# Kernel tuning notes

Measured on AMD Instinct MI355X. Metric: run time of the kernel, lower is better.

Reference implementation:

```python
import jax, jax.numpy as jnp
import numpy as np

B, S, D_IN, H, D_OUT = 2048, 16, 512, 1024, 64

def _lin_init(key, fan_in, fan_out):
    k1, k2 = jax.random.split(key)
    bound = 1.0 / np.sqrt(fan_in)
    W = jax.random.uniform(k1, (fan_in, fan_out), jnp.float32, -bound, bound)
    b = jax.random.uniform(k2, (fan_out,), jnp.float32, -bound, bound)
    return W, b

def setup_inputs() -> dict:
    key = jax.random.key(0)
    ks = jax.random.split(key, 7)
    x = jax.random.normal(ks[0], (B, S, D_IN), jnp.float32)
    Wi, bi = _lin_init(ks[1], D_IN, H)
    W1, b1 = _lin_init(ks[2], H, H)
    W2, b2 = _lin_init(ks[3], H, H)
    W3, b3 = _lin_init(ks[4], H, H)
    Wo1, bo1 = _lin_init(ks[5], H, H // 2)
    Wo2, bo2 = _lin_init(ks[6], H // 2, D_OUT)
    return {"x": x, "Wi": Wi, "bi": bi, "W1": W1, "b1": b1, "W2": W2, "b2": b2,
            "W3": W3, "b3": b3, "Wo1": Wo1, "bo1": bo1, "Wo2": Wo2, "bo2": bo2}

def reference(x, Wi, bi, W1, b1, W2, b2, W3, b3, Wo1, bo1, Wo2, bo2):
    seq_len = x.shape[1]
    dt = 1.0 / (seq_len - 1)  # t = linspace(0, 1, seq_len)

    def f(h):
        h = jax.nn.gelu(h @ W1 + b1, approximate=False)
        h = jax.nn.gelu(h @ W2 + b2, approximate=False)
        h = jax.nn.gelu(h @ W3 + b3, approximate=False)
        return h

    h0 = x[:, 0, :] @ Wi + bi  # [B, H]

    def rk4_38_step(h, _):  # torchdiffeq fixed-grid rk4 uses the 3/8 rule
        k1 = f(h)
        k2 = f(h + dt * k1 / 3.0)
        k3 = f(h + dt * (k2 - k1 / 3.0))
        k4 = f(h + dt * (k1 - k2 + k3))
        return h + dt * (k1 + 3.0 * k2 + 3.0 * k3 + k4) / 8.0, None

    h_final, _ = jax.lax.scan(rk4_38_step, h0, None, length=seq_len - 1)
    out = jax.nn.gelu(h_final @ Wo1 + bo1, approximate=False) @ Wo2 + bo2
    return out
```

## Files before the change

kernel.cpp:

```cpp
#include <hip/hip_runtime.h>
#include <hip/hip_bf16.h>
#include <math.h>

typedef __attribute__((ext_vector_type(8))) short bf16x8;
typedef __attribute__((ext_vector_type(4))) float f32x4;

#define EPI_T   0
#define EPI_H0  1
#define EPI_K1  2
#define EPI_K2  3
#define EPI_K3  4
#define EPI_K4  5
#define EPI_OUT 6

static __device__ __forceinline__ unsigned short f2bf(float f) {
  unsigned int u = __float_as_uint(f);
  u += 0x7FFFu + ((u >> 16) & 1u);
  return (unsigned short)(u >> 16);
}
static __device__ __forceinline__ float bf2f(unsigned short s) {
  return __uint_as_float(((unsigned int)s) << 16);
}
static __device__ __forceinline__ float gelu_f(float x) {
  return 0.5f * x * (1.0f + erff(x * 0.70710678118654752f));
}

typedef __attribute__((address_space(3))) unsigned int lds_u32;
typedef const __attribute__((address_space(1))) unsigned int glb_u32;
static __device__ __forceinline__ void gl_lds16(const unsigned short* g, unsigned short* l) {
  __builtin_amdgcn_global_load_lds((glb_u32*)g, (lds_u32*)l, 16, 0, 0);
}

template<int EPI>
__global__ __launch_bounds__(256, 2)
void gemm_k(const unsigned short* __restrict__ A,
            const unsigned short* __restrict__ Wt,
            const float* __restrict__ bias,
            void* __restrict__ outp,
            unsigned short* __restrict__ ob2,
            const float* __restrict__ hF,
            float* __restrict__ huF,
            const unsigned short* __restrict__ k1p,
            const unsigned short* __restrict__ k2p,
            float dt, int N, int K, int nwg)
{
  __shared__ __attribute__((aligned(16))) unsigned short As[3][64][128];

  const int bid = blockIdx.x;
  const int cpx = nwg >> 3;
  const int wid = (bid & 7) * cpx + (bid >> 3);
  const int nbx = N >> 6;
  const int bx = wid % nbx, by = wid / nbx;
  const int brow = by << 6, bcol = bx << 6;

  const int tid = threadIdx.x;
  const int lane = tid & 63;
  const int wv = tid >> 6;
  const int wr = wv >> 1, wc = wv & 1;
  const int l15 = lane & 15, l4 = lane >> 4;
  const int KT = K >> 7;

  f32x4 acc[2][2];
  const f32x4 zf = {0.f, 0.f, 0.f, 0.f};
#pragma unroll
  for (int m = 0; m < 2; ++m)
#pragma unroll
    for (int n = 0; n < 2; ++n) acc[m][n] = zf;

  const unsigned short* pB0 = Wt + (size_t)(bcol + wc * 32 + l15) * K + l4 * 8;
  const unsigned short* pB1 = pB0 + (size_t)16 * K;

  const int lrow = lane >> 4;
  auto STAGE = [&](int slot, int kt) {
    const int kof = kt << 7;
#pragma unroll
    for (int c = 0; c < 4; ++c) {
      const int r0 = wv * 16 + c * 4;
      const int sc = l15 ^ ((r0 + lrow) & 15);
      gl_lds16(A + (size_t)(brow + r0 + lrow) * K + kof + sc * 8, &As[slot][r0][0]);
    }
  };

  auto LOADB = [&](bf16x8 (&bg)[2][4], int kt) {
    const int kof = kt << 7;
#pragma unroll
    for (int ks = 0; ks < 4; ++ks) {
      bg[0][ks] = *(const bf16x8*)(pB0 + kof + ks * 32);
      bg[1][ks] = *(const bf16x8*)(pB1 + kof + ks * 32);
    }
  };

  auto COMP = [&](int slot, bf16x8 (&bg)[2][4]) {
    __builtin_amdgcn_s_setprio(1);
#pragma unroll
    for (int ks = 0; ks < 4; ++ks) {
      const int ch = ((ks * 4 + l4) ^ l15) * 8;
      bf16x8 af0 = *(const bf16x8*)&As[slot][wr * 32 + l15][ch];
      bf16x8 af1 = *(const bf16x8*)&As[slot][wr * 32 + 16 + l15][ch];
      acc[0][0] = __builtin_amdgcn_mfma_f32_16x16x32_bf16(af0, bg[0][ks], acc[0][0], 0, 0, 0);
      acc[0][1] = __builtin_amdgcn_mfma_f32_16x16x32_bf16(af0, bg[1][ks], acc[0][1], 0, 0, 0);
      acc[1][0] = __builtin_amdgcn_mfma_f32_16x16x32_bf16(af1, bg[0][ks], acc[1][0], 0, 0, 0);
      acc[1][1] = __builtin_amdgcn_mfma_f32_16x16x32_bf16(af1, bg[1][ks], acc[1][1], 0, 0, 0);
    }
    __builtin_amdgcn_s_setprio(0);
  };

  bf16x8 Bp[2][4], Bq[2][4];

  STAGE(0, 0);
  STAGE(1, 1);
  LOADB(Bp, 0);

  auto body = [&](int t, bf16x8 (&cur)[2][4], bf16x8 (&nxt)[2][4]) {
    if (t + 1 < KT) { asm volatile("s_waitcnt vmcnt(4)" ::: "memory"); }
    else            { asm volatile("s_waitcnt vmcnt(0)" ::: "memory"); }
    __builtin_amdgcn_s_barrier();
    __builtin_amdgcn_sched_barrier(0);
    if (t + 1 < KT) LOADB(nxt, t + 1);
    COMP(t % 3, cur);
    if (t + 2 < KT) STAGE((t + 2) % 3, t + 2);
  };

  for (int t = 0; t < KT; t += 2) {
    body(t, Bp, Bq);
    body(t + 1, Bq, Bp);
  }

  const float dt3 = dt * (1.f / 3.f), dt8 = dt * 0.125f, dt38 = dt * 0.375f;
#pragma unroll
  for (int n = 0; n < 2; ++n) {
    const int col = bcol + wc * 32 + n * 16 + l15;
    const float bv = bias[col];
#pragma unroll
    for (int m = 0; m < 2; ++m) {
      const int r0 = brow + wr * 32 + m * 16 + l4 * 4;
#pragma unroll
      for (int r = 0; r < 4; ++r) {
        const int row = r0 + r;
        const float a = acc[m][n][r] + bv;
        const size_t ix = (size_t)row * N + col;
        const size_t ih = (size_t)row * 1024 + col;
        if constexpr (EPI == EPI_T) {
          ((unsigned short*)outp)[ix] = f2bf(gelu_f(a));
        } else if constexpr (EPI == EPI_H0) {
          ((float*)outp)[ix] = a;
          ob2[ix] = f2bf(a);
        } else if constexpr (EPI == EPI_K1) {
          const float k1 = gelu_f(a);
          const float h = hF[ih];
          ((unsigned short*)outp)[ih] = f2bf(k1);
          huF[ih] = h + dt8 * k1;
          ob2[ih] = f2bf(h + dt3 * k1);
        } else if constexpr (EPI == EPI_K2) {
          const float k2 = gelu_f(a);
          const float h = hF[ih];
          const float k1 = bf2f(k1p[ih]);
          ((unsigned short*)outp)[ih] = f2bf(k2);
          huF[ih] += dt38 * k2;
          ob2[ih] = f2bf(h - dt3 * k1 + dt * k2);
        } else if constexpr (EPI == EPI_K3) {
          const float k3 = gelu_f(a);
          const float h = hF[ih];
          const float k1 = bf2f(k1p[ih]);
          const float k2 = bf2f(k2p[ih]);
          huF[ih] += dt38 * k3;
          ob2[ih] = f2bf(h + dt * (k1 - k2 + k3));
        } else if constexpr (EPI == EPI_K4) {
          const float k4 = gelu_f(a);
          const float hn = huF[ih] + dt8 * k4;
          ((float*)outp)[ih] = hn;
          ob2[ih] = f2bf(hn);
        } else {
          ((float*)outp)[ix] = a;
        }
      }
    }
  }
}

__global__ void transpose_k(const float* __restrict__ W, unsigned short* __restrict__ Wt,
                            int K, int N) {
  __shared__ float tile[32][33];
  const int n0 = blockIdx.x * 32, k0 = blockIdx.y * 32;
  const int lx = threadIdx.x, ly = threadIdx.y;
#pragma unroll
  for (int r = ly; r < 32; r += 8)
    tile[r][lx] = W[(size_t)(k0 + r) * N + n0 + lx];
  __syncthreads();
#pragma unroll
  for (int r = ly; r < 32; r += 8)
    Wt[(size_t)(n0 + r) * K + k0 + lx] = f2bf(tile[lx][r]);
}

__global__ void convx_k(const float* __restrict__ x, unsigned short* __restrict__ xb) {
  const int r = blockIdx.x;
  const int c = threadIdx.x << 3;
  const float* s = x + (size_t)r * 8192 + c;
  f32x4 u0 = *(const f32x4*)s;
  f32x4 u1 = *(const f32x4*)(s + 4);
  union { unsigned short q[8]; bf16x8 v; } t;
#pragma unroll
  for (int j = 0; j < 4; ++j) { t.q[j] = f2bf(u0[j]); t.q[4 + j] = f2bf(u1[j]); }
  *(bf16x8*)(xb + (size_t)r * 512 + c) = t.v;
}

template<int EPI>
static inline void G(hipStream_t st, const void* A, const unsigned short* Wt,
                     const float* bias, void* out, void* ob2,
                     const float* hF, float* huF,
                     const unsigned short* k1p, const unsigned short* k2p,
                     float dt, int N, int K) {
  const int nwg = (2048 / 64) * (N / 64);
  gemm_k<EPI><<<nwg, 256, 0, st>>>((const unsigned short*)A, Wt, bias, out,
                                   (unsigned short*)ob2, hF, huF, k1p, k2p, dt, N, K, nwg);
}

extern "C" void kernel_launch(void* const* d_in, const int* in_sizes, int n_in,
                              void* d_out, int out_size, void* d_ws, size_t ws_size,
                              hipStream_t stream) {
  const float* x   = (const float*)d_in[0];
  const float* Wi  = (const float*)d_in[1];
  const float* bi  = (const float*)d_in[2];
  const float* W1  = (const float*)d_in[3];
  const float* b1  = (const float*)d_in[4];
  const float* W2  = (const float*)d_in[5];
  const float* b2  = (const float*)d_in[6];
  const float* W3  = (const float*)d_in[7];
  const float* b3  = (const float*)d_in[8];
  const float* Wo1 = (const float*)d_in[9];
  const float* bo1 = (const float*)d_in[10];
  const float* Wo2 = (const float*)d_in[11];
  const float* bo2 = (const float*)d_in[12];

  char* ws = (char*)d_ws;
  unsigned short* Wti  = (unsigned short*)(ws + (0ull  << 20));
  unsigned short* Wt1  = (unsigned short*)(ws + (1ull  << 20));
  unsigned short* Wt2  = (unsigned short*)(ws + (3ull  << 20));
  unsigned short* Wt3  = (unsigned short*)(ws + (5ull  << 20));
  unsigned short* Wto1 = (unsigned short*)(ws + (7ull  << 20));
  unsigned short* Wto2 = (unsigned short*)(ws + (8ull  << 20));
  float*          h    = (float*)(ws + (9ull  << 20));
  float*          hu   = (float*)(ws + (17ull << 20));
  unsigned short* xb   = (unsigned short*)hu;
  unsigned short* k1b  = (unsigned short*)(ws + (25ull << 20));
  unsigned short* o1b  = k1b;
  unsigned short* k2b  = (unsigned short*)(ws + (29ull << 20));
  unsigned short* t1b  = (unsigned short*)(ws + (33ull << 20));
  unsigned short* t2b  = (unsigned short*)(ws + (37ull << 20));
  unsigned short* cA   = (unsigned short*)(ws + (41ull << 20));
  unsigned short* hb   = (unsigned short*)(ws + (45ull << 20));

  dim3 tb(32, 8);
  transpose_k<<<dim3(1024 / 32,  512 / 32), tb, 0, stream>>>(Wi,  Wti,  512, 1024);
  transpose_k<<<dim3(1024 / 32, 1024 / 32), tb, 0, stream>>>(W1,  Wt1, 1024, 1024);
  transpose_k<<<dim3(1024 / 32, 1024 / 32), tb, 0, stream>>>(W2,  Wt2, 1024, 1024);
  transpose_k<<<dim3(1024 / 32, 1024 / 32), tb, 0, stream>>>(W3,  Wt3, 1024, 1024);
  transpose_k<<<dim3( 512 / 32, 1024 / 32), tb, 0, stream>>>(Wo1, Wto1, 1024, 512);
  transpose_k<<<dim3(  64 / 32,  512 / 32), tb, 0, stream>>>(Wo2, Wto2,  512,  64);
  convx_k<<<2048, 64, 0, stream>>>(x, xb);

  const float dt = 1.0f / 15.0f;

  G<EPI_H0>(stream, xb, Wti, bi, h, hb, nullptr, nullptr, nullptr, nullptr, dt, 1024, 512);

  for (int s = 0; s < 15; ++s) {
    G<EPI_T >(stream, hb,  Wt1, b1, t1b, nullptr, nullptr, nullptr, nullptr, nullptr, dt, 1024, 1024);
    G<EPI_T >(stream, t1b, Wt2, b2, t2b, nullptr, nullptr, nullptr, nullptr, nullptr, dt, 1024, 1024);
    G<EPI_K1>(stream, t2b, Wt3, b3, k1b, cA, h, hu, nullptr, nullptr, dt, 1024, 1024);
    G<EPI_T >(stream, cA,  Wt1, b1, t1b, nullptr, nullptr, nullptr, nullptr, nullptr, dt, 1024, 1024);
    G<EPI_T >(stream, t1b, Wt2, b2, t2b, nullptr, nullptr, nullptr, nullptr, nullptr, dt, 1024, 1024);
    G<EPI_K2>(stream, t2b, Wt3, b3, k2b, cA, h, hu, k1b, nullptr, dt, 1024, 1024);
    G<EPI_T >(stream, cA,  Wt1, b1, t1b, nullptr, nullptr, nullptr, nullptr, nullptr, dt, 1024, 1024);
    G<EPI_T >(stream, t1b, Wt2, b2, t2b, nullptr, nullptr, nullptr, nullptr, nullptr, dt, 1024, 1024);
    G<EPI_K3>(stream, t2b, Wt3, b3, nullptr, cA, h, hu, k1b, k2b, dt, 1024, 1024);
    G<EPI_T >(stream, cA,  Wt1, b1, t1b, nullptr, nullptr, nullptr, nullptr, nullptr, dt, 1024, 1024);
    G<EPI_T >(stream, t1b, Wt2, b2, t2b, nullptr, nullptr, nullptr, nullptr, nullptr, dt, 1024, 1024);
    G<EPI_K4>(stream, t2b, Wt3, b3, h, hb, nullptr, hu, nullptr, nullptr, dt, 1024, 1024);
  }

  G<EPI_T  >(stream, hb,  Wto1, bo1, o1b, nullptr, nullptr, nullptr, nullptr, nullptr, dt, 512, 1024);
  G<EPI_OUT>(stream, o1b, Wto2, bo2, d_out, nullptr, nullptr, nullptr, nullptr, nullptr, dt, 64, 512);
}
```

Measured before the change: 4.153 ms.

## Replace per-GEMM launches with a persistent kernel using row-group atomic barriers

The 181 separate GEMM launches of the ODE integration become one persistent kernel of 256 workgroups. Each workgroup owns a 64x128 output tile and loops over all RK4 phases. Only the 8 workgroups sharing a row block depend on each other, so phases are ordered by per-row-block atomic counters instead of kernel boundaries. The goal is to remove launch and tail overhead and allow row groups to drift apart. In exchange it depends on all 256 workgroups being co-resident, since otherwise the spin-wait can deadlock, and it uses a smaller 64-wide K tile with 512-thread blocks at one block per CU.

```diff
diff --git a/kernel.cpp b/kernel.cpp
--- a/kernel.cpp
+++ b/kernel.cpp
@@ -13,6 +13,8 @@
 #define EPI_K4  5
 #define EPI_OUT 6
 
+template<int E> struct Tag { static constexpr int value = E; };
+
 static __device__ __forceinline__ unsigned short f2bf(float f) {
   unsigned int u = __float_as_uint(f);
   u += 0x7FFFu + ((u >> 16) & 1u);
@@ -29,6 +31,172 @@
 typedef const __attribute__((address_space(1))) unsigned int glb_u32;
 static __device__ __forceinline__ void gl_lds16(const unsigned short* g, unsigned short* l) {
   __builtin_amdgcn_global_load_lds((glb_u32*)g, (lds_u32*)l, 16, 0, 0);
+}
+
+__global__ __launch_bounds__(512, 1)
+void ode_persist(const unsigned short* __restrict__ xb,
+                 const unsigned short* __restrict__ Wti, const float* __restrict__ bi,
+                 const unsigned short* __restrict__ Wt1, const float* __restrict__ b1,
+                 const unsigned short* __restrict__ Wt2, const float* __restrict__ b2,
+                 const unsigned short* __restrict__ Wt3, const float* __restrict__ b3,
+                 float* __restrict__ h, float* __restrict__ hu,
+                 unsigned short* __restrict__ hb, unsigned short* __restrict__ cA,
+                 unsigned short* __restrict__ k1b, unsigned short* __restrict__ k2b,
+                 unsigned short* __restrict__ t1b, unsigned short* __restrict__ t2b,
+                 unsigned int* __restrict__ ctr, float dt)
+{
+  __shared__ __attribute__((aligned(16))) unsigned short As[12][64][64];
+
+  const int bid = blockIdx.x;
+  const int by = bid >> 3, bx = bid & 7;
+  const int brow = by << 6, bcol = bx << 7;
+  const int tid  = threadIdx.x;
+  const int lane = tid & 63;
+  const int wv   = tid >> 6;
+  const int wr   = wv >> 2, wc = wv & 3;
+  const int l15  = lane & 15, l4 = lane >> 4;
+  const int rr   = tid >> 3;
+  const int cc   = tid & 7;
+  const int sch  = cc ^ (rr & 7);
+
+  const float dt3 = dt * (1.f / 3.f), dt8 = dt * 0.125f, dt38 = dt * 0.375f;
+  unsigned int goal = 0;
+
+  auto bar = [&]() {
+    goal += 8;
+    __syncthreads();
+    if (tid == 0) {
+      __hip_atomic_fetch_add(&ctr[by], 1u, __ATOMIC_RELEASE, __HIP_MEMORY_SCOPE_AGENT);
+      while (__hip_atomic_load(&ctr[by], __ATOMIC_ACQUIRE, __HIP_MEMORY_SCOPE_AGENT) < goal)
+        __builtin_amdgcn_s_sleep(8);
+    }
+    __syncthreads();
+  };
+
+  auto gphase = [&](auto epi_c, const unsigned short* Aptr, int lda, int Kp,
+                    const unsigned short* Wt, const float* bias,
+                    unsigned short* outT) {
+    constexpr int EPI = decltype(epi_c)::value;
+    const int KT = Kp >> 6;
+    const unsigned short* pB0 = Wt + (size_t)(bcol + wc * 32 + l15) * Kp + l4 * 8;
+    const unsigned short* pB1 = pB0 + (size_t)16 * Kp;
+
+    f32x4 acc[2][2];
+    const f32x4 zf = {0.f, 0.f, 0.f, 0.f};
+#pragma unroll
+    for (int m = 0; m < 2; ++m)
+#pragma unroll
+      for (int n = 0; n < 2; ++n) acc[m][n] = zf;
+
+    auto STAGE = [&](int slot, int t) {
+      gl_lds16(Aptr + (size_t)(brow + rr) * lda + (t << 6) + sch * 8,
+               &As[slot][wv * 8][0]);
+    };
+    auto LOADB = [&](bf16x8 (&bg)[2][2], int t) {
+      const int kof = t << 6;
+      bg[0][0] = *(const bf16x8*)(pB0 + kof);
+      bg[0][1] = *(const bf16x8*)(pB0 + kof + 32);
+      bg[1][0] = *(const bf16x8*)(pB1 + kof);
+      bg[1][1] = *(const bf16x8*)(pB1 + kof + 32);
+    };
+    auto COMP = [&](int slot, bf16x8 (&bg)[2][2]) {
+      const int tr0 = wr * 32 + l15;
+      const int xr  = tr0 & 7;
+      __builtin_amdgcn_s_setprio(1);
+#pragma unroll
+      for (int ks = 0; ks < 2; ++ks) {
+        const int ch = (((ks << 2) + l4) ^ xr) << 3;
+        bf16x8 af0 = *(const bf16x8*)&As[slot][tr0][ch];
+        bf16x8 af1 = *(const bf16x8*)&As[slot][tr0 + 16][ch];
+        acc[0][0] = __builtin_amdgcn_mfma_f32_16x16x32_bf16(af0, bg[0][ks], acc[0][0], 0, 0, 0);
+        acc[0][1] = __builtin_amdgcn_mfma_f32_16x16x32_bf16(af0, bg[1][ks], acc[0][1], 0, 0, 0);
+        acc[1][0] = __builtin_amdgcn_mfma_f32_16x16x32_bf16(af1, bg[0][ks], acc[1][0], 0, 0, 0);
+        acc[1][1] = __builtin_amdgcn_mfma_f32_16x16x32_bf16(af1, bg[1][ks], acc[1][1], 0, 0, 0);
+      }
+      __builtin_amdgcn_s_setprio(0);
+    };
+
+    bf16x8 Bp[2][2], Bq[2][2];
+    STAGE(0, 0);
+    STAGE(1, 1);
+    LOADB(Bp, 0);
+
+    auto body = [&](int t, bf16x8 (&cur)[2][2], bf16x8 (&nxt)[2][2]) {
+      if (t + 1 < KT) { asm volatile("s_waitcnt vmcnt(1)" ::: "memory"); }
+      else            { asm volatile("s_waitcnt vmcnt(0)" ::: "memory"); }
+      __builtin_amdgcn_s_barrier();
+      __builtin_amdgcn_sched_barrier(0);
+      if (t + 1 < KT) LOADB(nxt, t + 1);
+      COMP(t % 3, cur);
+      if (t + 2 < KT) STAGE((t + 2) % 3, t + 2);
+    };
+    for (int t = 0; t < KT; t += 2) {
+      body(t, Bp, Bq);
+      body(t + 1, Bq, Bp);
+    }
+
+#pragma unroll
+    for (int n = 0; n < 2; ++n) {
+      const int col = bcol + wc * 32 + n * 16 + l15;
+      const float bv = bias[col];
+#pragma unroll
+      for (int m = 0; m < 2; ++m) {
+        const int r0 = brow + wr * 32 + m * 16 + l4 * 4;
+#pragma unroll
+        for (int r = 0; r < 4; ++r) {
+          const size_t ih = (size_t)(r0 + r) * 1024 + col;
+          const float a = acc[m][n][r] + bv;
+          if constexpr (EPI == EPI_T) {
+            outT[ih] = f2bf(gelu_f(a));
+          } else if constexpr (EPI == EPI_H0) {
+            h[ih] = a;
+            hb[ih] = f2bf(a);
+          } else if constexpr (EPI == EPI_K1) {
+            const float k1 = gelu_f(a);
+            const float hv = h[ih];
+            k1b[ih] = f2bf(k1);
+            hu[ih] = hv + dt8 * k1;
+            cA[ih] = f2bf(hv + dt3 * k1);
+          } else if constexpr (EPI == EPI_K2) {
+            const float k2 = gelu_f(a);
+            const float hv = h[ih];
+            const float k1 = bf2f(k1b[ih]);
+            k2b[ih] = f2bf(k2);
+            hu[ih] += dt38 * k2;
+            cA[ih] = f2bf(hv - dt3 * k1 + dt * k2);
+          } else if constexpr (EPI == EPI_K3) {
+            const float k3 = gelu_f(a);
+            const float hv = h[ih];
+            const float k1 = bf2f(k1b[ih]);
+            const float k2 = bf2f(k2b[ih]);
+            hu[ih] += dt38 * k3;
+            cA[ih] = f2bf(hv + dt * (k1 - k2 + k3));
+          } else if constexpr (EPI == EPI_K4) {
+            const float k4 = gelu_f(a);
+            const float hn = hu[ih] + dt8 * k4;
+            h[ih] = hn;
+            hb[ih] = f2bf(hn);
+          }
+        }
+      }
+    }
+  };
+
+  gphase(Tag<EPI_H0>{}, xb, 512, 512, Wti, bi, nullptr); bar();
+  for (int s = 0; s < 15; ++s) {
+    gphase(Tag<EPI_T >{}, hb,  1024, 1024, Wt1, b1, t1b); bar();
+    gphase(Tag<EPI_T >{}, t1b, 1024, 1024, Wt2, b2, t2b); bar();
+    gphase(Tag<EPI_K1>{}, t2b, 1024, 1024, Wt3, b3, nullptr); bar();
+    gphase(Tag<EPI_T >{}, cA,  1024, 1024, Wt1, b1, t1b); bar();
+    gphase(Tag<EPI_T >{}, t1b, 1024, 1024, Wt2, b2, t2b); bar();
+    gphase(Tag<EPI_K2>{}, t2b, 1024, 1024, Wt3, b3, nullptr); bar();
+    gphase(Tag<EPI_T >{}, cA,  1024, 1024, Wt1, b1, t1b); bar();
+    gphase(Tag<EPI_T >{}, t1b, 1024, 1024, Wt2, b2, t2b); bar();
+    gphase(Tag<EPI_K3>{}, t2b, 1024, 1024, Wt3, b3, nullptr); bar();
+    gphase(Tag<EPI_T >{}, cA,  1024, 1024, Wt1, b1, t1b); bar();
+    gphase(Tag<EPI_T >{}, t1b, 1024, 1024, Wt2, b2, t2b); bar();
+    gphase(Tag<EPI_K4>{}, t2b, 1024, 1024, Wt3, b3, nullptr); bar();
+  }
 }
 
 template<int EPI>
@@ -37,12 +205,7 @@
             const unsigned short* __restrict__ Wt,
             const float* __restrict__ bias,
             void* __restrict__ outp,
-            unsigned short* __restrict__ ob2,
-            const float* __restrict__ hF,
-            float* __restrict__ huF,
-            const unsigned short* __restrict__ k1p,
-            const unsigned short* __restrict__ k2p,
-            float dt, int N, int K, int nwg)
+            int N, int K, int nwg)
 {
   __shared__ __attribute__((aligned(16))) unsigned short As[3][64][128];
 
@@ -80,7 +243,6 @@
       gl_lds16(A + (size_t)(brow + r0 + lrow) * K + kof + sc * 8, &As[slot][r0][0]);
     }
   };
-
   auto LOADB = [&](bf16x8 (&bg)[2][4], int kt) {
     const int kof = kt << 7;
 #pragma unroll
@@ -89,7 +251,6 @@
       bg[1][ks] = *(const bf16x8*)(pB1 + kof + ks * 32);
     }
   };
-
   auto COMP = [&](int slot, bf16x8 (&bg)[2][4]) {
     __builtin_amdgcn_s_setprio(1);
 #pragma unroll
@@ -106,11 +267,9 @@
   };
 
   bf16x8 Bp[2][4], Bq[2][4];
-
   STAGE(0, 0);
   STAGE(1, 1);
   LOADB(Bp, 0);
-
   auto body = [&](int t, bf16x8 (&cur)[2][4], bf16x8 (&nxt)[2][4]) {
     if (t + 1 < KT) { asm volatile("s_waitcnt vmcnt(4)" ::: "memory"); }
     else            { asm volatile("s_waitcnt vmcnt(0)" ::: "memory"); }
@@ -120,13 +279,11 @@
     COMP(t % 3, cur);
     if (t + 2 < KT) STAGE((t + 2) % 3, t + 2);
   };
-
   for (int t = 0; t < KT; t += 2) {
     body(t, Bp, Bq);
     body(t + 1, Bq, Bp);
   }
 
-  const float dt3 = dt * (1.f / 3.f), dt8 = dt * 0.125f, dt38 = dt * 0.375f;
 #pragma unroll
   for (int n = 0; n < 2; ++n) {
     const int col = bcol + wc * 32 + n * 16 + l15;
@@ -136,43 +293,10 @@
       const int r0 = brow + wr * 32 + m * 16 + l4 * 4;
 #pragma unroll
       for (int r = 0; r < 4; ++r) {
-        const int row = r0 + r;
+        const size_t ix = (size_t)(r0 + r) * N + col;
         const float a = acc[m][n][r] + bv;
-        const size_t ix = (size_t)row * N + col;
-        const size_t ih = (size_t)row * 1024 + col;
-        if constexpr (EPI == EPI_T) {
-          ((unsigned short*)outp)[ix] = f2bf(gelu_f(a));
-        } else if constexpr (EPI == EPI_H0) {
-          ((float*)outp)[ix] = a;
-          ob2[ix] = f2bf(a);
-        } else if constexpr (EPI == EPI_K1) {
-          const float k1 = gelu_f(a);
-          const float h = hF[ih];
-          ((unsigned short*)outp)[ih] = f2bf(k1);
-          huF[ih] = h + dt8 * k1;
-          ob2[ih] = f2bf(h + dt3 * k1);
-        } else if constexpr (EPI == EPI_K2) {
-          const float k2 = gelu_f(a);
-          const float h = hF[ih];
-          const float k1 = bf2f(k1p[ih]);
-          ((unsigned short*)outp)[ih] = f2bf(k2);
-          huF[ih] += dt38 * k2;
-          ob2[ih] = f2bf(h - dt3 * k1 + dt * k2);
-        } else if constexpr (EPI == EPI_K3) {
-          const float k3 = gelu_f(a);
-          const float h = hF[ih];
-          const float k1 = bf2f(k1p[ih]);
-          const float k2 = bf2f(k2p[ih]);
-          huF[ih] += dt38 * k3;
-          ob2[ih] = f2bf(h + dt * (k1 - k2 + k3));
-        } else if constexpr (EPI == EPI_K4) {
-          const float k4 = gelu_f(a);
-          const float hn = huF[ih] + dt8 * k4;
-          ((float*)outp)[ih] = hn;
-          ob2[ih] = f2bf(hn);
-        } else {
-          ((float*)outp)[ix] = a;
-        }
+        if constexpr (EPI == EPI_T) ((unsigned short*)outp)[ix] = f2bf(gelu_f(a));
+        else                        ((float*)outp)[ix] = a;
       }
     }
   }
@@ -202,17 +326,6 @@
 #pragma unroll
   for (int j = 0; j < 4; ++j) { t.q[j] = f2bf(u0[j]); t.q[4 + j] = f2bf(u1[j]); }
   *(bf16x8*)(xb + (size_t)r * 512 + c) = t.v;
-}
-
-template<int EPI>
-static inline void G(hipStream_t st, const void* A, const unsigned short* Wt,
-                     const float* bias, void* out, void* ob2,
-                     const float* hF, float* huF,
-                     const unsigned short* k1p, const unsigned short* k2p,
-                     float dt, int N, int K) {
-  const int nwg = (2048 / 64) * (N / 64);
-  gemm_k<EPI><<<nwg, 256, 0, st>>>((const unsigned short*)A, Wt, bias, out,
-                                   (unsigned short*)ob2, hF, huF, k1p, k2p, dt, N, K, nwg);
 }
 
 extern "C" void kernel_launch(void* const* d_in, const int* in_sizes, int n_in,
@@ -249,6 +362,7 @@
   unsigned short* t2b  = (unsigned short*)(ws + (37ull << 20));
   unsigned short* cA   = (unsigned short*)(ws + (41ull << 20));
   unsigned short* hb   = (unsigned short*)(ws + (45ull << 20));
+  unsigned int*   ctr  = (unsigned int*)(ws + (49ull << 20));
 
   dim3 tb(32, 8);
   transpose_k<<<dim3(1024 / 32,  512 / 32), tb, 0, stream>>>(Wi,  Wti,  512, 1024);
@@ -258,26 +372,17 @@
   transpose_k<<<dim3( 512 / 32, 1024 / 32), tb, 0, stream>>>(Wo1, Wto1, 1024, 512);
   transpose_k<<<dim3(  64 / 32,  512 / 32), tb, 0, stream>>>(Wo2, Wto2,  512,  64);
   convx_k<<<2048, 64, 0, stream>>>(x, xb);
+  hipMemsetAsync(ctr, 0, 32 * sizeof(unsigned int), stream);
 
   const float dt = 1.0f / 15.0f;
 
-  G<EPI_H0>(stream, xb, Wti, bi, h, hb, nullptr, nullptr, nullptr, nullptr, dt, 1024, 512);
-
-  for (int s = 0; s < 15; ++s) {
-    G<EPI_T >(stream, hb,  Wt1, b1, t1b, nullptr, nullptr, nullptr, nullptr, nullptr, dt, 1024, 1024);
-    G<EPI_T >(stream, t1b, Wt2, b2, t2b, nullptr, nullptr, nullptr, nullptr, nullptr, dt, 1024, 1024);
-    G<EPI_K1>(stream, t2b, Wt3, b3, k1b, cA, h, hu, nullptr, nullptr, dt, 1024, 1024);
-    G<EPI_T >(stream, cA,  Wt1, b1, t1b, nullptr, nullptr, nullptr, nullptr, nullptr, dt, 1024, 1024);
-    G<EPI_T >(stream, t1b, Wt2, b2, t2b, nullptr, nullptr, nullptr, nullptr, nullptr, dt, 1024, 1024);
-    G<EPI_K2>(stream, t2b, Wt3, b3, k2b, cA, h, hu, k1b, nullptr, dt, 1024, 1024);
-    G<EPI_T >(stream, cA,  Wt1, b1, t1b, nullptr, nullptr, nullptr, nullptr, nullptr, dt, 1024, 1024);
-    G<EPI_T >(stream, t1b, Wt2, b2, t2b, nullptr, nullptr, nullptr, nullptr, nullptr, dt, 1024, 1024);
-    G<EPI_K3>(stream, t2b, Wt3, b3, nullptr, cA, h, hu, k1b, k2b, dt, 1024, 1024);
-    G<EPI_T >(stream, cA,  Wt1, b1, t1b, nullptr, nullptr, nullptr, nullptr, nullptr, dt, 1024, 1024);
-    G<EPI_T >(stream, t1b, Wt2, b2, t2b, nullptr, nullptr, nullptr, nullptr, nullptr, dt, 1024, 1024);
-    G<EPI_K4>(stream, t2b, Wt3, b3, h, hb, nullptr, hu, nullptr, nullptr, dt, 1024, 1024);
+  ode_persist<<<256, 512, 0, stream>>>(xb, Wti, bi, Wt1, b1, Wt2, b2, Wt3, b3,
+                                       h, hu, hb, cA, k1b, k2b, t1b, t2b, ctr, dt);
+
+  {
+    const int nwg1 = (2048 / 64) * (512 / 64);
+    gemm_k<EPI_T><<<nwg1, 256, 0, stream>>>(hb, Wto1, bo1, o1b, 512, 1024, nwg1);
+    const int nwg2 = (2048 / 64) * (64 / 64);
+    gemm_k<EPI_OUT><<<nwg2, 256, 0, stream>>>(o1b, Wto2, bo2, d_out, 64, 512, nwg2);
   }
-
-  G<EPI_T  >(stream, hb,  Wto1, bo1, o1b, nullptr, nullptr, nullptr, nullptr, nullptr, dt, 512, 1024);
-  G<EPI_OUT>(stream, o1b, Wto2, bo2, d_out, nullptr, nullptr, nullptr, nullptr, nullptr, dt, 64, 512);
-}
+}
```

New measurement: 7.282 ms. +75.3%, slower.

## Shrink GEMM tiles to 64x32 with 64-wide K steps and raise occupancy

Applied to the files above, without the earlier changes.

Each GEMM workgroup now computes a 64x32 output tile instead of 64x64, and the K loop steps 64 at a time instead of 128. Each wave owns a 16-row strip, and the LDS swizzle and the waitcnt accounting are adjusted to match. The launch grid doubles and launch bounds ask for 4 blocks per CU, so more workgroups are in flight to hide latency on these small M=2048 GEMMs. In exchange, each tile reuses its A and B operands less, so more global and LDS traffic is spent per MFMA.

```diff
diff --git a/kernel.cpp b/kernel.cpp
--- a/kernel.cpp
+++ b/kernel.cpp
@@ -32,7 +32,7 @@
 }
 
 template<int EPI>
-__global__ __launch_bounds__(256, 2)
+__global__ __launch_bounds__(256, 4)
 void gemm_k(const unsigned short* __restrict__ A,
             const unsigned short* __restrict__ Wt,
             const float* __restrict__ bias,
@@ -44,75 +44,68 @@
             const unsigned short* __restrict__ k2p,
             float dt, int N, int K, int nwg)
 {
-  __shared__ __attribute__((aligned(16))) unsigned short As[3][64][128];
+  __shared__ __attribute__((aligned(16))) unsigned short As[3][64][64];
 
   const int bid = blockIdx.x;
   const int cpx = nwg >> 3;
   const int wid = (bid & 7) * cpx + (bid >> 3);
-  const int nbx = N >> 6;
+  const int nbx = N >> 5;
   const int bx = wid % nbx, by = wid / nbx;
-  const int brow = by << 6, bcol = bx << 6;
-
-  const int tid = threadIdx.x;
+  const int brow = by << 6, bcol = bx << 5;
+
+  const int tid  = threadIdx.x;
   const int lane = tid & 63;
-  const int wv = tid >> 6;
-  const int wr = wv >> 1, wc = wv & 1;
-  const int l15 = lane & 15, l4 = lane >> 4;
-  const int KT = K >> 7;
-
-  f32x4 acc[2][2];
+  const int wv   = tid >> 6;
+  const int l15  = lane & 15, l4 = lane >> 4;
+  const int srow = lane >> 3;
+  const int sch  = lane & 7;
+  const int KT   = K >> 6;
+
+  f32x4 acc[2];
   const f32x4 zf = {0.f, 0.f, 0.f, 0.f};
-#pragma unroll
-  for (int m = 0; m < 2; ++m)
-#pragma unroll
-    for (int n = 0; n < 2; ++n) acc[m][n] = zf;
-
-  const unsigned short* pB0 = Wt + (size_t)(bcol + wc * 32 + l15) * K + l4 * 8;
+  acc[0] = zf; acc[1] = zf;
+
+  const unsigned short* pB0 = Wt + (size_t)(bcol + l15) * K + l4 * 8;
   const unsigned short* pB1 = pB0 + (size_t)16 * K;
 
-  const int lrow = lane >> 4;
-  auto STAGE = [&](int slot, int kt) {
-    const int kof = kt << 7;
-#pragma unroll
-    for (int c = 0; c < 4; ++c) {
-      const int r0 = wv * 16 + c * 4;
-      const int sc = l15 ^ ((r0 + lrow) & 15);
-      gl_lds16(A + (size_t)(brow + r0 + lrow) * K + kof + sc * 8, &As[slot][r0][0]);
+  auto STAGE = [&](int slot, int t) {
+    const int kof = t << 6;
+#pragma unroll
+    for (int c = 0; c < 2; ++c) {
+      const int r0 = c * 32 + wv * 8;
+      const int row = r0 + srow;
+      const int sc = sch ^ (row & 7);
+      gl_lds16(A + (size_t)(brow + row) * K + kof + sc * 8, &As[slot][r0][0]);
     }
   };
-
-  auto LOADB = [&](bf16x8 (&bg)[2][4], int kt) {
-    const int kof = kt << 7;
-#pragma unroll
-    for (int ks = 0; ks < 4; ++ks) {
-      bg[0][ks] = *(const bf16x8*)(pB0 + kof + ks * 32);
-      bg[1][ks] = *(const bf16x8*)(pB1 + kof + ks * 32);
-    }
-  };
-
-  auto COMP = [&](int slot, bf16x8 (&bg)[2][4]) {
+  auto LOADB = [&](bf16x8 (&bg)[2][2], int t) {
+    const int kof = t << 6;
+    bg[0][0] = *(const bf16x8*)(pB0 + kof);
+    bg[0][1] = *(const bf16x8*)(pB0 + kof + 32);
+    bg[1][0] = *(const bf16x8*)(pB1 + kof);
+    bg[1][1] = *(const bf16x8*)(pB1 + kof + 32);
+  };
+  auto COMP = [&](int slot, bf16x8 (&bg)[2][2]) {
+    const int r = wv * 16 + l15;
+    const int xr = l15 & 7;
     __builtin_amdgcn_s_setprio(1);
 #pragma unroll
-    for (int ks = 0; ks < 4; ++ks) {
-      const int ch = ((ks * 4 + l4) ^ l15) * 8;
-      bf16x8 af0 = *(const bf16x8*)&As[slot][wr * 32 + l15][ch];
-      bf16x8 af1 = *(const bf16x8*)&As[slot][wr * 32 + 16 + l15][ch];
-      acc[0][0] = __builtin_amdgcn_mfma_f32_16x16x32_bf16(af0, bg[0][ks], acc[0][0], 0, 0, 0);
-      acc[0][1] = __builtin_amdgcn_mfma_f32_16x16x32_bf16(af0, bg[1][ks], acc[0][1], 0, 0, 0);
-      acc[1][0] = __builtin_amdgcn_mfma_f32_16x16x32_bf16(af1, bg[0][ks], acc[1][0], 0, 0, 0);
-      acc[1][1] = __builtin_amdgcn_mfma_f32_16x16x32_bf16(af1, bg[1][ks], acc[1][1], 0, 0, 0);
+    for (int ks = 0; ks < 2; ++ks) {
+      const int ch = (((ks << 2) + l4) ^ xr) << 3;
+      bf16x8 af = *(const bf16x8*)&As[slot][r][ch];
+      acc[0] = __builtin_amdgcn_mfma_f32_16x16x32_bf16(af, bg[0][ks], acc[0], 0, 0, 0);
+      acc[1] = __builtin_amdgcn_mfma_f32_16x16x32_bf16(af, bg[1][ks], acc[1], 0, 0, 0);
     }
     __builtin_amdgcn_s_setprio(0);
   };
 
-  bf16x8 Bp[2][4], Bq[2][4];
-
+  bf16x8 Bp[2][2], Bq[2][2];
   STAGE(0, 0);
+  LOADB(Bp, 0);
   STAGE(1, 1);
-  LOADB(Bp, 0);
-
-  auto body = [&](int t, bf16x8 (&cur)[2][4], bf16x8 (&nxt)[2][4]) {
-    if (t + 1 < KT) { asm volatile("s_waitcnt vmcnt(4)" ::: "memory"); }
+
+  auto body = [&](int t, bf16x8 (&cur)[2][2], bf16x8 (&nxt)[2][2]) {
+    if (t + 1 < KT) { asm volatile("s_waitcnt vmcnt(2)" ::: "memory"); }
     else            { asm volatile("s_waitcnt vmcnt(0)" ::: "memory"); }
     __builtin_amdgcn_s_barrier();
     __builtin_amdgcn_sched_barrier(0);
@@ -120,7 +113,6 @@
     COMP(t % 3, cur);
     if (t + 2 < KT) STAGE((t + 2) % 3, t + 2);
   };
-
   for (int t = 0; t < KT; t += 2) {
     body(t, Bp, Bq);
     body(t + 1, Bq, Bp);
@@ -129,50 +121,47 @@
   const float dt3 = dt * (1.f / 3.f), dt8 = dt * 0.125f, dt38 = dt * 0.375f;
 #pragma unroll
   for (int n = 0; n < 2; ++n) {
-    const int col = bcol + wc * 32 + n * 16 + l15;
+    const int col = bcol + n * 16 + l15;
     const float bv = bias[col];
-#pragma unroll
-    for (int m = 0; m < 2; ++m) {
-      const int r0 = brow + wr * 32 + m * 16 + l4 * 4;
-#pragma unroll
-      for (int r = 0; r < 4; ++r) {
-        const int row = r0 + r;
-        const float a = acc[m][n][r] + bv;
-        const size_t ix = (size_t)row * N + col;
-        const size_t ih = (size_t)row * 1024 + col;
-        if constexpr (EPI == EPI_T) {
-          ((unsigned short*)outp)[ix] = f2bf(gelu_f(a));
-        } else if constexpr (EPI == EPI_H0) {
-          ((float*)outp)[ix] = a;
-          ob2[ix] = f2bf(a);
-        } else if constexpr (EPI == EPI_K1) {
-          const float k1 = gelu_f(a);
-          const float h = hF[ih];
-          ((unsigned short*)outp)[ih] = f2bf(k1);
-          huF[ih] = h + dt8 * k1;
-          ob2[ih] = f2bf(h + dt3 * k1);
-        } else if constexpr (EPI == EPI_K2) {
-          const float k2 = gelu_f(a);
-          const float h = hF[ih];
-          const float k1 = bf2f(k1p[ih]);
-          ((unsigned short*)outp)[ih] = f2bf(k2);
-          huF[ih] += dt38 * k2;
-          ob2[ih] = f2bf(h - dt3 * k1 + dt * k2);
-        } else if constexpr (EPI == EPI_K3) {
-          const float k3 = gelu_f(a);
-          const float h = hF[ih];
-          const float k1 = bf2f(k1p[ih]);
-          const float k2 = bf2f(k2p[ih]);
-          huF[ih] += dt38 * k3;
-          ob2[ih] = f2bf(h + dt * (k1 - k2 + k3));
-        } else if constexpr (EPI == EPI_K4) {
-          const float k4 = gelu_f(a);
-          const float hn = huF[ih] + dt8 * k4;
-          ((float*)outp)[ih] = hn;
-          ob2[ih] = f2bf(hn);
-        } else {
-          ((float*)outp)[ix] = a;
-        }
+    const int r0 = brow + wv * 16 + l4 * 4;
+#pragma unroll
+    for (int r = 0; r < 4; ++r) {
+      const int row = r0 + r;
+      const float a = acc[n][r] + bv;
+      const size_t ix = (size_t)row * N + col;
+      const size_t ih = (size_t)row * 1024 + col;
+      if constexpr (EPI == EPI_T) {
+        ((unsigned short*)outp)[ix] = f2bf(gelu_f(a));
+      } else if constexpr (EPI == EPI_H0) {
+        ((float*)outp)[ix] = a;
+        ob2[ix] = f2bf(a);
+      } else if constexpr (EPI == EPI_K1) {
+        const float k1 = gelu_f(a);
+        const float hv = hF[ih];
+        ((unsigned short*)outp)[ih] = f2bf(k1);
+        huF[ih] = hv + dt8 * k1;
+        ob2[ih] = f2bf(hv + dt3 * k1);
+      } else if constexpr (EPI == EPI_K2) {
+        const float k2 = gelu_f(a);
+        const float hv = hF[ih];
+        const float k1 = bf2f(k1p[ih]);
+        ((unsigned short*)outp)[ih] = f2bf(k2);
+        huF[ih] += dt38 * k2;
+        ob2[ih] = f2bf(hv - dt3 * k1 + dt * k2);
+      } else if constexpr (EPI == EPI_K3) {
+        const float k3 = gelu_f(a);
+        const float hv = hF[ih];
+        const float k1 = bf2f(k1p[ih]);
+        const float k2 = bf2f(k2p[ih]);
+        huF[ih] += dt38 * k3;
+        ob2[ih] = f2bf(hv + dt * (k1 - k2 + k3));
+      } else if constexpr (EPI == EPI_K4) {
+        const float k4 = gelu_f(a);
+        const float hn = huF[ih] + dt8 * k4;
+        ((float*)outp)[ih] = hn;
+        ob2[ih] = f2bf(hn);
+      } else {
+        ((float*)outp)[ix] = a;
       }
     }
   }
@@ -210,7 +199,7 @@
                      const float* hF, float* huF,
                      const unsigned short* k1p, const unsigned short* k2p,
                      float dt, int N, int K) {
-  const int nwg = (2048 / 64) * (N / 64);
+  const int nwg = (2048 / 64) * (N / 32);
   gemm_k<EPI><<<nwg, 256, 0, st>>>((const unsigned short*)A, Wt, bias, out,
                                    (unsigned short*)ob2, hF, huF, k1p, k2p, dt, N, K, nwg);
 }
```

After: 6.726 ms. 1.62x slower.
